# Optimization experiments

Hardware: AMD Instinct MI355X
Metric: run time of the kernel (lower is better)

The kernel has to match this reference:

```python
import jax, jax.numpy as jnp
import numpy as np


def _lstm(x, W, U, b, return_sequences):
    # x: [B,T,F]; W: [F,4H]; U: [H,4H]; b: [4H]. Keras gate order: i,f,c,o.
    B = x.shape[0]
    H = U.shape[0]
    # precompute input projection for all timesteps: [T,B,4H]
    xW = jnp.einsum('btf,fg->tbg', x, W) + b
    h0 = jnp.zeros((B, H), x.dtype)
    c0 = jnp.zeros((B, H), x.dtype)

    def step(carry, xw):
        h, c = carry
        z = xw + h @ U  # [B,4H]
        i, f, g, o = jnp.split(z, 4, axis=-1)
        i = jax.nn.sigmoid(i)
        f = jax.nn.sigmoid(f)
        g = jax.nn.relu(g)      # activation='relu' on candidate
        o = jax.nn.sigmoid(o)
        c = f * c + i * g
        h = o * jax.nn.relu(c)  # activation='relu' on cell output
        return (h, c), h

    (hT, _), hs = jax.lax.scan(step, (h0, c0), xW)
    if return_sequences:
        return jnp.transpose(hs, (1, 0, 2))  # [B,T,H]
    return hT  # [B,H]


def setup_inputs() -> dict:
    key = jax.random.key(0)
    ks = jax.random.split(key, 11)
    B, T, F = 512, 512, 64
    H1, H2, D1, D2 = 128, 64, 25, 1
    s = 0.05  # small weight scale keeps the relu-LSTM recurrence numerically stable
    return {
        'x':   jax.random.normal(ks[0], (B, T, F), jnp.float32),
        'W1':  jax.random.normal(ks[1], (F, 4 * H1), jnp.float32) * s,
        'U1':  jax.random.normal(ks[2], (H1, 4 * H1), jnp.float32) * s,
        'b1':  jnp.zeros((4 * H1,), jnp.float32),
        'W2':  jax.random.normal(ks[3], (H1, 4 * H2), jnp.float32) * s,
        'U2':  jax.random.normal(ks[4], (H2, 4 * H2), jnp.float32) * s,
        'b2':  jnp.zeros((4 * H2,), jnp.float32),
        'Wd1': jax.random.normal(ks[5], (H2, D1), jnp.float32) * s,
        'bd1': jnp.zeros((D1,), jnp.float32),
        'Wd2': jax.random.normal(ks[6], (D1, D2), jnp.float32) * s,
        'bd2': jnp.zeros((D2,), jnp.float32),
    }


def reference(x, W1, U1, b1, W2, U2, b2, Wd1, bd1, Wd2, bd2):
    h = _lstm(x, W1, U1, b1, return_sequences=True)   # [B,T,128]
    h = _lstm(h, W2, U2, b2, return_sequences=False)  # [B,64]
    h = h @ Wd1 + bd1                                  # [B,25]
    return h @ Wd2 + bd2                               # [B,1]
```

## Files before the change

### kernel.cpp

```cpp
#include <hip/hip_runtime.h>
#include <type_traits>

typedef _Float16 f16;
typedef _Float16 f16x4 __attribute__((ext_vector_type(4)));
typedef _Float16 f16x8 __attribute__((ext_vector_type(8)));
typedef float    f32x4 __attribute__((ext_vector_type(4)));

constexpr int TT = 512;
constexpr int FF = 64;
constexpr int H1 = 128;
constexpr int H2 = 64;
constexpr int D1 = 25;
constexpr int S1 = 136;
constexpr int S2 = 72;
constexpr int XC = 8;
constexpr float L2E = 1.44269504088896f;

__device__ __forceinline__ float sigm2(float z) {
    return __builtin_amdgcn_rcpf(1.f + __builtin_amdgcn_exp2f(-z));
}

__device__ __forceinline__ f32x4 mfma16(f16x8 a, f16x8 b, f32x4 c) {
    return __builtin_amdgcn_mfma_f32_16x16x32_f16(a, b, c, 0, 0, 0);
}

__device__ __forceinline__ void gl_lds16(const f16* g, f16* l) {
    __builtin_amdgcn_global_load_lds(
        (const __attribute__((address_space(1))) unsigned int*)g,
        (__attribute__((address_space(3))) unsigned int*)l, 16, 0, 0);
}

__global__ void cvt_x_kernel(const float* __restrict__ x, f16* __restrict__ xh) {
    const size_t i = ((size_t)blockIdx.x * blockDim.x + threadIdx.x) * 4;
    const float4 v = *(const float4*)(x + i);
    f16x4 h; h[0] = (f16)v.x; h[1] = (f16)v.y; h[2] = (f16)v.z; h[3] = (f16)v.w;
    *(f16x4*)(xh + i) = h;
}

__global__ __launch_bounds__(768, 3)
void lstm_pipe9(const f16* __restrict__ xh, const float* __restrict__ W1,
                const float* __restrict__ U1, const float* __restrict__ b1,
                const float* __restrict__ W2, const float* __restrict__ U2,
                const float* __restrict__ b2, const float* __restrict__ Wd1,
                const float* __restrict__ bd1,const float* __restrict__ Wd2,
                const float* __restrict__ bd2, float* __restrict__ out)
{
    const int tid  = threadIdx.x;
    const int w    = tid >> 6;
    const int lane = tid & 63;
    const int quad = lane >> 4;
    const int lid  = lane & 15;
    const int b0   = blockIdx.x * 16;
    const bool isL1 = (w < 8);
    const int  j    = isL1 ? w : (w - 8);

    __shared__ __align__(16) f16 h1b[2][16][S1];
    __shared__ __align__(16) f16 h2b[2][16][S2];
    __shared__ __align__(16) f16 xlds[2][XC * 8 * 16 * 8];
    __shared__ float h2f[16][H2];
    __shared__ float dsh[16][D1];

    for (int i = tid; i < 2 * 16 * S1 / 2; i += 768) ((unsigned*)h1b)[i] = 0u;
    for (int i = tid; i < 2 * 16 * S2 / 2; i += 768) ((unsigned*)h2b)[i] = 0u;

    for (int s = tid; s < XC * 8 * 16; s += 768) {
        const int tl = s >> 7, fs = (s >> 4) & 7, row = s & 15;
        const f16* gp = xh + ((size_t)(b0 + row) * TT + tl) * FF + fs * 8;
        gl_lds16(gp, &xlds[0][(s >> 6) * 512]);
    }

    f16x8 wt[4][6];
    f32x4 bsp[4];
    float cs[4] = {0.f, 0.f, 0.f, 0.f};

    if (isL1) {
#pragma unroll
        for (int g = 0; g < 4; ++g) {
            const float sc = (g == 2) ? 1.f : L2E;
            const int n = 128 * g + 16 * w + lid;
#pragma unroll
            for (int rr = 0; rr < 4; ++rr)
                bsp[g][rr] = b1[128 * g + 16 * w + quad * 4 + rr] * sc;
#pragma unroll
            for (int c = 0; c < 4; ++c) {
                f16x8 f;
#pragma unroll
                for (int e = 0; e < 8; ++e)
                    f[e] = (f16)(U1[(32 * c + quad * 8 + e) * 512 + n] * sc);
                wt[g][c] = f;
            }
#pragma unroll
            for (int c = 0; c < 2; ++c) {
                f16x8 f;
#pragma unroll
                for (int e = 0; e < 8; ++e)
                    f[e] = (f16)(W1[(32 * c + quad * 8 + e) * 512 + n] * sc);
                wt[g][4 + c] = f;
            }
        }
    } else {
#pragma unroll
        for (int g = 0; g < 4; ++g) {
            const float sc = (g == 2) ? 1.f : L2E;
            const int n = 64 * g + 16 * j + lid;
#pragma unroll
            for (int rr = 0; rr < 4; ++rr)
                bsp[g][rr] = b2[64 * g + 16 * j + quad * 4 + rr] * sc;
#pragma unroll
            for (int c = 0; c < 4; ++c) {
                f16x8 f;
#pragma unroll
                for (int e = 0; e < 8; ++e)
                    f[e] = (f16)(W2[(32 * c + quad * 8 + e) * 256 + n] * sc);
                wt[g][c] = f;
            }
#pragma unroll
            for (int c = 0; c < 2; ++c) {
                f16x8 f;
#pragma unroll
                for (int e = 0; e < 8; ++e)
                    f[e] = (f16)(U2[(32 * c + quad * 8 + e) * 256 + n] * sc);
                wt[g][4 + c] = f;
            }
        }
    }
    __syncthreads();

    auto step = [&](auto parc, int i) {
        constexpr int PAR = decltype(parc)::value;
        constexpr int PR = PAR ^ 1;
        constexpr int PW = PAR;
        constexpr int QR = PAR;
        constexpr int QW = PAR ^ 1;
        if (isL1) {
            const f16* xc = &xlds[(i >> 3) & 1][(i & 7) * 1024];
            f16x8 fr0 = *(const f16x8*)&h1b[PR][lid][quad * 8];
            f16x8 fr1 = *(const f16x8*)&h1b[PR][lid][32 + quad * 8];
            f16x8 fr2 = *(const f16x8*)&h1b[PR][lid][64 + quad * 8];
            f16x8 fr3 = *(const f16x8*)&h1b[PR][lid][96 + quad * 8];
            f16x8 xf0 = *(const f16x8*)&xc[(quad * 16 + lid) * 8];
            f16x8 xf1 = *(const f16x8*)&xc[((4 + quad) * 16 + lid) * 8];
            f32x4 acc[4];
#pragma unroll
            for (int g = 0; g < 4; ++g) {
                f32x4 a = mfma16(wt[g][0], fr0, bsp[g]);
                a = mfma16(wt[g][1], fr1, a);
                a = mfma16(wt[g][2], fr2, a);
                a = mfma16(wt[g][3], fr3, a);
                a = mfma16(wt[g][4], xf0, a);
                a = mfma16(wt[g][5], xf1, a);
                acc[g] = a;
            }
            f16x4 hp;
#pragma unroll
            for (int r = 0; r < 4; ++r) {
                const float ig = sigm2(acc[0][r]);
                const float fg = sigm2(acc[1][r]);
                const float gg = fmaxf(acc[2][r], 0.f);
                const float og = sigm2(acc[3][r]);
                const float cc = fg * cs[r] + ig * gg;
                cs[r] = cc;
                hp[r] = (f16)(og * fmaxf(cc, 0.f));
            }
            *(f16x4*)&h1b[PW][lid][16 * w + quad * 4] = hp;
        } else {
            if (i >= 1) {
                f16x8 fr0 = *(const f16x8*)&h1b[PR][lid][quad * 8];
                f16x8 fr1 = *(const f16x8*)&h1b[PR][lid][32 + quad * 8];
                f16x8 fr2 = *(const f16x8*)&h1b[PR][lid][64 + quad * 8];
                f16x8 fr3 = *(const f16x8*)&h1b[PR][lid][96 + quad * 8];
                f16x8 fr4 = *(const f16x8*)&h2b[QR][lid][quad * 8];
                f16x8 fr5 = *(const f16x8*)&h2b[QR][lid][32 + quad * 8];
                f32x4 acc[4];
#pragma unroll
                for (int g = 0; g < 4; ++g) {
                    f32x4 a = mfma16(wt[g][0], fr0, bsp[g]);
                    a = mfma16(wt[g][1], fr1, a);
                    a = mfma16(wt[g][2], fr2, a);
                    a = mfma16(wt[g][3], fr3, a);
                    a = mfma16(wt[g][4], fr4, a);
                    a = mfma16(wt[g][5], fr5, a);
                    acc[g] = a;
                }
                f16x4 hp;
#pragma unroll
                for (int r = 0; r < 4; ++r) {
                    const float ig = sigm2(acc[0][r]);
                    const float fg = sigm2(acc[1][r]);
                    const float gg = fmaxf(acc[2][r], 0.f);
                    const float og = sigm2(acc[3][r]);
                    const float cc = fg * cs[r] + ig * gg;
                    cs[r] = cc;
                    hp[r] = (f16)(og * fmaxf(cc, 0.f));
                }
                *(f16x4*)&h2b[QW][lid][16 * j + quad * 4] = hp;
            }
        }
    };

    for (int ii = 0; ii < TT; ii += 2) {
        if ((ii & (XC - 1)) == 0 && ii + XC < TT) {
            const int nc = (ii >> 3) + 1;
            f16* dst = xlds[nc & 1];
            for (int s = tid; s < XC * 8 * 16; s += 768) {
                const int tl = s >> 7, fs = (s >> 4) & 7, row = s & 15;
                const f16* gp = xh + ((size_t)(b0 + row) * TT + (nc * XC + tl)) * FF + fs * 8;
                gl_lds16(gp, &dst[(s >> 6) * 512]);
            }
        }
        step(std::integral_constant<int, 0>{}, ii);
        __syncthreads();
        step(std::integral_constant<int, 1>{}, ii + 1);
        __syncthreads();
    }

    if (!isL1) {
        f16x8 fr0 = *(const f16x8*)&h1b[1][lid][quad * 8];
        f16x8 fr1 = *(const f16x8*)&h1b[1][lid][32 + quad * 8];
        f16x8 fr2 = *(const f16x8*)&h1b[1][lid][64 + quad * 8];
        f16x8 fr3 = *(const f16x8*)&h1b[1][lid][96 + quad * 8];
        f16x8 fr4 = *(const f16x8*)&h2b[0][lid][quad * 8];
        f16x8 fr5 = *(const f16x8*)&h2b[0][lid][32 + quad * 8];
        f32x4 acc[4];
#pragma unroll
        for (int g = 0; g < 4; ++g) {
            f32x4 a = mfma16(wt[g][0], fr0, bsp[g]);
            a = mfma16(wt[g][1], fr1, a);
            a = mfma16(wt[g][2], fr2, a);
            a = mfma16(wt[g][3], fr3, a);
            a = mfma16(wt[g][4], fr4, a);
            a = mfma16(wt[g][5], fr5, a);
            acc[g] = a;
        }
        float4 ho;
#pragma unroll
        for (int r = 0; r < 4; ++r) {
            const float ig = sigm2(acc[0][r]);
            const float fg = sigm2(acc[1][r]);
            const float gg = fmaxf(acc[2][r], 0.f);
            const float og = sigm2(acc[3][r]);
            const float cc = fg * cs[r] + ig * gg;
            (&ho.x)[r] = og * fmaxf(cc, 0.f);
        }
        *(float4*)&h2f[lid][16 * j + quad * 4] = ho;
    }
    __syncthreads();

    for (int idx = tid; idx < 16 * D1; idx += 768) {
        const int bq = idx / D1, p = idx % D1;
        float d = bd1[p];
#pragma unroll
        for (int k = 0; k < H2; ++k) d += h2f[bq][k] * Wd1[k * D1 + p];
        dsh[bq][p] = d * Wd2[p];
    }
    __syncthreads();
    if (tid < 16) {
        float o = bd2[0];
#pragma unroll
        for (int p = 0; p < D1; ++p) o += dsh[tid][p];
        out[b0 + tid] = o;
    }
}

extern "C" void kernel_launch(void* const* d_in, const int* in_sizes, int n_in,
                              void* d_out, int out_size, void* d_ws, size_t ws_size,
                              hipStream_t stream) {
    (void)in_sizes; (void)n_in; (void)out_size; (void)ws_size;
    const float* x   = (const float*)d_in[0];
    const float* W1  = (const float*)d_in[1];
    const float* U1  = (const float*)d_in[2];
    const float* b1  = (const float*)d_in[3];
    const float* W2  = (const float*)d_in[4];
    const float* U2  = (const float*)d_in[5];
    const float* b2  = (const float*)d_in[6];
    const float* Wd1 = (const float*)d_in[7];
    const float* bd1 = (const float*)d_in[8];
    const float* Wd2 = (const float*)d_in[9];
    const float* bd2 = (const float*)d_in[10];
    float* out = (float*)d_out;
    f16*   xh  = (f16*)d_ws;

    const int nx = 512 * 512 * 64;
    cvt_x_kernel<<<dim3(nx / (256 * 4)), dim3(256), 0, stream>>>(x, xh);
    lstm_pipe9<<<dim3(32), dim3(768), 0, stream>>>(
        xh, W1, U1, b1, W2, U2, b2, Wd1, bd1, Wd2, bd2, out);
}
```

Baseline: 714.2 us.

## Precompute layer-1 input projection in a parallel GEMM kernel before recurrence

Adds a separate highly parallel kernel that computes x*W1+b1 for every timestep and stores it in fp16, in an MFMA-fragment-friendly layout in workspace. The recurrent kernel then only does the U1 matmul per step and prefetches the next step's projection from global memory. This moves the input-projection work off the serial 32-block recurrence and onto the whole GPU. The cost is a 256MB intermediate write and read. The new path runs only when the workspace is large enough, otherwise it falls back to the old path.

Measured after the change: 842.9 us. 1.18x slower.

```diff
diff --git a/kernel.cpp b/kernel.cpp
--- a/kernel.cpp
+++ b/kernel.cpp
@@ -28,6 +28,282 @@
     __builtin_amdgcn_global_load_lds(
         (const __attribute__((address_space(1))) unsigned int*)g,
         (__attribute__((address_space(3))) unsigned int*)l, 16, 0, 0);
+}
+
+__device__ __forceinline__ size_t xw_off(int bg, int t, int w, int quad, int lid) {
+    return ((((size_t)(bg * 512 + t) * 8 + w) * 4 + quad) * 16 + lid) * 16;
+}
+
+__global__ __launch_bounds__(512, 4)
+void xw_gemm(const float* __restrict__ x, const float* __restrict__ W1,
+             const float* __restrict__ b1, f16* __restrict__ xw)
+{
+    const int tid  = threadIdx.x;
+    const int w    = tid >> 6;
+    const int lane = tid & 63;
+    const int quad = lane >> 4;
+    const int lid  = lane & 15;
+    const int bg   = blockIdx.x & 31;
+    const int tc   = blockIdx.x >> 5;
+
+    f16x8 wa[4][2];
+    f32x4 bsp[4];
+#pragma unroll
+    for (int g = 0; g < 4; ++g) {
+        const float sc = (g == 2) ? 1.f : L2E;
+        const int n = 128 * g + 16 * w + lid;
+#pragma unroll
+        for (int rr = 0; rr < 4; ++rr)
+            bsp[g][rr] = b1[128 * g + 16 * w + quad * 4 + rr] * sc;
+#pragma unroll
+        for (int c = 0; c < 2; ++c) {
+            f16x8 f;
+#pragma unroll
+            for (int e = 0; e < 8; ++e)
+                f[e] = (f16)(W1[(32 * c + quad * 8 + e) * 512 + n] * sc);
+            wa[g][c] = f;
+        }
+    }
+
+    for (int tt = 0; tt < 8; ++tt) {
+        const int t = tc * 8 + tt;
+        const float* xr = x + ((size_t)(bg * 16 + lid) * TT + t) * FF + quad * 8;
+        const float4 p0 = *(const float4*)xr;
+        const float4 p1 = *(const float4*)(xr + 4);
+        const float4 p2 = *(const float4*)(xr + 32);
+        const float4 p3 = *(const float4*)(xr + 36);
+        f16x8 xb0, xb1;
+        xb0[0]=(f16)p0.x; xb0[1]=(f16)p0.y; xb0[2]=(f16)p0.z; xb0[3]=(f16)p0.w;
+        xb0[4]=(f16)p1.x; xb0[5]=(f16)p1.y; xb0[6]=(f16)p1.z; xb0[7]=(f16)p1.w;
+        xb1[0]=(f16)p2.x; xb1[1]=(f16)p2.y; xb1[2]=(f16)p2.z; xb1[3]=(f16)p2.w;
+        xb1[4]=(f16)p3.x; xb1[5]=(f16)p3.y; xb1[6]=(f16)p3.z; xb1[7]=(f16)p3.w;
+
+        f32x4 acc[4];
+#pragma unroll
+        for (int g = 0; g < 4; ++g) {
+            f32x4 a = mfma16(wa[g][0], xb0, bsp[g]);
+            acc[g] = mfma16(wa[g][1], xb1, a);
+        }
+        f16x8 s01, s23;
+#pragma unroll
+        for (int r = 0; r < 4; ++r) {
+            s01[r]     = (f16)acc[0][r];
+            s01[4 + r] = (f16)acc[1][r];
+            s23[r]     = (f16)acc[2][r];
+            s23[4 + r] = (f16)acc[3][r];
+        }
+        f16* dst = xw + xw_off(bg, t, w, quad, lid);
+        *(f16x8*)dst = s01;
+        *(f16x8*)(dst + 8) = s23;
+    }
+}
+
+__global__ __launch_bounds__(768, 3)
+void lstm_pipe10(const f16* __restrict__ xw, const float* __restrict__ U1,
+                 const float* __restrict__ W2, const float* __restrict__ U2,
+                 const float* __restrict__ b2, const float* __restrict__ Wd1,
+                 const float* __restrict__ bd1,const float* __restrict__ Wd2,
+                 const float* __restrict__ bd2, float* __restrict__ out)
+{
+    const int tid  = threadIdx.x;
+    const int w    = tid >> 6;
+    const int lane = tid & 63;
+    const int quad = lane >> 4;
+    const int lid  = lane & 15;
+    const int bg   = blockIdx.x;
+    const int b0   = bg * 16;
+    const bool isL1 = (w < 8);
+    const int  j    = isL1 ? w : (w - 8);
+
+    __shared__ __align__(16) f16 h1b[2][16][S1];
+    __shared__ __align__(16) f16 h2b[2][16][S2];
+    __shared__ float h2f[16][H2];
+    __shared__ float dsh[16][D1];
+
+    for (int i = tid; i < 2 * 16 * S1 / 2; i += 768) ((unsigned*)h1b)[i] = 0u;
+    for (int i = tid; i < 2 * 16 * S2 / 2; i += 768) ((unsigned*)h2b)[i] = 0u;
+
+    f16x8 wt[4][6];
+    f32x4 bsp[4];
+    float cs[4] = {0.f, 0.f, 0.f, 0.f};
+    f16x8 xw01, xw23;
+
+    if (isL1) {
+#pragma unroll
+        for (int g = 0; g < 4; ++g) {
+            const float sc = (g == 2) ? 1.f : L2E;
+            const int n = 128 * g + 16 * w + lid;
+#pragma unroll
+            for (int c = 0; c < 4; ++c) {
+                f16x8 f;
+#pragma unroll
+                for (int e = 0; e < 8; ++e)
+                    f[e] = (f16)(U1[(32 * c + quad * 8 + e) * 512 + n] * sc);
+                wt[g][c] = f;
+            }
+        }
+        const f16* p0 = xw + xw_off(bg, 0, w, quad, lid);
+        xw01 = *(const f16x8*)p0;
+        xw23 = *(const f16x8*)(p0 + 8);
+    } else {
+#pragma unroll
+        for (int g = 0; g < 4; ++g) {
+            const float sc = (g == 2) ? 1.f : L2E;
+            const int n = 64 * g + 16 * j + lid;
+#pragma unroll
+            for (int rr = 0; rr < 4; ++rr)
+                bsp[g][rr] = b2[64 * g + 16 * j + quad * 4 + rr] * sc;
+#pragma unroll
+            for (int c = 0; c < 4; ++c) {
+                f16x8 f;
+#pragma unroll
+                for (int e = 0; e < 8; ++e)
+                    f[e] = (f16)(W2[(32 * c + quad * 8 + e) * 256 + n] * sc);
+                wt[g][c] = f;
+            }
+#pragma unroll
+            for (int c = 0; c < 2; ++c) {
+                f16x8 f;
+#pragma unroll
+                for (int e = 0; e < 8; ++e)
+                    f[e] = (f16)(U2[(32 * c + quad * 8 + e) * 256 + n] * sc);
+                wt[g][4 + c] = f;
+            }
+        }
+    }
+    __syncthreads();
+
+    auto step = [&](auto parc, int i) {
+        constexpr int PAR = decltype(parc)::value;
+        constexpr int PR = PAR ^ 1;
+        constexpr int PW = PAR;
+        constexpr int QR = PAR;
+        constexpr int QW = PAR ^ 1;
+        if (isL1) {
+            f16x8 fr0 = *(const f16x8*)&h1b[PR][lid][quad * 8];
+            f16x8 fr1 = *(const f16x8*)&h1b[PR][lid][32 + quad * 8];
+            f16x8 fr2 = *(const f16x8*)&h1b[PR][lid][64 + quad * 8];
+            f16x8 fr3 = *(const f16x8*)&h1b[PR][lid][96 + quad * 8];
+            f32x4 acc[4];
+#pragma unroll
+            for (int r = 0; r < 4; ++r) {
+                acc[0][r] = (float)xw01[r];
+                acc[1][r] = (float)xw01[4 + r];
+                acc[2][r] = (float)xw23[r];
+                acc[3][r] = (float)xw23[4 + r];
+            }
+            if (i + 1 < TT) {
+                const f16* p = xw + xw_off(bg, i + 1, w, quad, lid);
+                xw01 = *(const f16x8*)p;
+                xw23 = *(const f16x8*)(p + 8);
+            }
+#pragma unroll
+            for (int g = 0; g < 4; ++g) {
+                acc[g] = mfma16(wt[g][0], fr0, acc[g]);
+                acc[g] = mfma16(wt[g][1], fr1, acc[g]);
+                acc[g] = mfma16(wt[g][2], fr2, acc[g]);
+                acc[g] = mfma16(wt[g][3], fr3, acc[g]);
+            }
+            f16x4 hp;
+#pragma unroll
+            for (int r = 0; r < 4; ++r) {
+                const float ig = sigm2(acc[0][r]);
+                const float fg = sigm2(acc[1][r]);
+                const float gg = fmaxf(acc[2][r], 0.f);
+                const float og = sigm2(acc[3][r]);
+                const float cc = fg * cs[r] + ig * gg;
+                cs[r] = cc;
+                hp[r] = (f16)(og * fmaxf(cc, 0.f));
+            }
+            *(f16x4*)&h1b[PW][lid][16 * w + quad * 4] = hp;
+        } else {
+            if (i >= 1) {
+                f16x8 fr0 = *(const f16x8*)&h1b[PR][lid][quad * 8];
+                f16x8 fr1 = *(const f16x8*)&h1b[PR][lid][32 + quad * 8];
+                f16x8 fr2 = *(const f16x8*)&h1b[PR][lid][64 + quad * 8];
+                f16x8 fr3 = *(const f16x8*)&h1b[PR][lid][96 + quad * 8];
+                f16x8 fr4 = *(const f16x8*)&h2b[QR][lid][quad * 8];
+                f16x8 fr5 = *(const f16x8*)&h2b[QR][lid][32 + quad * 8];
+                f32x4 acc[4];
+#pragma unroll
+                for (int g = 0; g < 4; ++g) {
+                    f32x4 a = mfma16(wt[g][0], fr0, bsp[g]);
+                    a = mfma16(wt[g][1], fr1, a);
+                    a = mfma16(wt[g][2], fr2, a);
+                    a = mfma16(wt[g][3], fr3, a);
+                    a = mfma16(wt[g][4], fr4, a);
+                    a = mfma16(wt[g][5], fr5, a);
+                    acc[g] = a;
+                }
+                f16x4 hp;
+#pragma unroll
+                for (int r = 0; r < 4; ++r) {
+                    const float ig = sigm2(acc[0][r]);
+                    const float fg = sigm2(acc[1][r]);
+                    const float gg = fmaxf(acc[2][r], 0.f);
+                    const float og = sigm2(acc[3][r]);
+                    const float cc = fg * cs[r] + ig * gg;
+                    cs[r] = cc;
+                    hp[r] = (f16)(og * fmaxf(cc, 0.f));
+                }
+                *(f16x4*)&h2b[QW][lid][16 * j + quad * 4] = hp;
+            }
+        }
+    };
+
+    for (int ii = 0; ii < TT; ii += 2) {
+        step(std::integral_constant<int, 0>{}, ii);
+        __syncthreads();
+        step(std::integral_constant<int, 1>{}, ii + 1);
+        __syncthreads();
+    }
+
+    if (!isL1) {
+        f16x8 fr0 = *(const f16x8*)&h1b[1][lid][quad * 8];
+        f16x8 fr1 = *(const f16x8*)&h1b[1][lid][32 + quad * 8];
+        f16x8 fr2 = *(const f16x8*)&h1b[1][lid][64 + quad * 8];
+        f16x8 fr3 = *(const f16x8*)&h1b[1][lid][96 + quad * 8];
+        f16x8 fr4 = *(const f16x8*)&h2b[0][lid][quad * 8];
+        f16x8 fr5 = *(const f16x8*)&h2b[0][lid][32 + quad * 8];
+        f32x4 acc[4];
+#pragma unroll
+        for (int g = 0; g < 4; ++g) {
+            f32x4 a = mfma16(wt[g][0], fr0, bsp[g]);
+            a = mfma16(wt[g][1], fr1, a);
+            a = mfma16(wt[g][2], fr2, a);
+            a = mfma16(wt[g][3], fr3, a);
+            a = mfma16(wt[g][4], fr4, a);
+            a = mfma16(wt[g][5], fr5, a);
+            acc[g] = a;
+        }
+        float4 ho;
+#pragma unroll
+        for (int r = 0; r < 4; ++r) {
+            const float ig = sigm2(acc[0][r]);
+            const float fg = sigm2(acc[1][r]);
+            const float gg = fmaxf(acc[2][r], 0.f);
+            const float og = sigm2(acc[3][r]);
+            const float cc = fg * cs[r] + ig * gg;
+            (&ho.x)[r] = og * fmaxf(cc, 0.f);
+        }
+        *(float4*)&h2f[lid][16 * j + quad * 4] = ho;
+    }
+    __syncthreads();
+
+    for (int idx = tid; idx < 16 * D1; idx += 768) {
+        const int bq = idx / D1, p = idx % D1;
+        float d = bd1[p];
+#pragma unroll
+        for (int k = 0; k < H2; ++k) d += h2f[bq][k] * Wd1[k * D1 + p];
+        dsh[bq][p] = d * Wd2[p];
+    }
+    __syncthreads();
+    if (tid < 16) {
+        float o = bd2[0];
+#pragma unroll
+        for (int p = 0; p < D1; ++p) o += dsh[tid][p];
+        out[b0 + tid] = o;
+    }
 }
 
 __global__ void cvt_x_kernel(const float* __restrict__ x, f16* __restrict__ xh) {
@@ -265,7 +541,7 @@
 extern "C" void kernel_launch(void* const* d_in, const int* in_sizes, int n_in,
                               void* d_out, int out_size, void* d_ws, size_t ws_size,
                               hipStream_t stream) {
-    (void)in_sizes; (void)n_in; (void)out_size; (void)ws_size;
+    (void)in_sizes; (void)n_in; (void)out_size;
     const float* x   = (const float*)d_in[0];
     const float* W1  = (const float*)d_in[1];
     const float* U1  = (const float*)d_in[2];
@@ -278,10 +554,18 @@
     const float* Wd2 = (const float*)d_in[9];
     const float* bd2 = (const float*)d_in[10];
     float* out = (float*)d_out;
-    f16*   xh  = (f16*)d_ws;
-
-    const int nx = 512 * 512 * 64;
-    cvt_x_kernel<<<dim3(nx / (256 * 4)), dim3(256), 0, stream>>>(x, xh);
-    lstm_pipe9<<<dim3(32), dim3(768), 0, stream>>>(
-        xh, W1, U1, b1, W2, U2, b2, Wd1, bd1, Wd2, bd2, out);
-}
+
+    const size_t need = (size_t)512 * 512 * 512 * sizeof(f16);
+    if (ws_size >= need) {
+        f16* xwbuf = (f16*)d_ws;
+        xw_gemm<<<dim3(2048), dim3(512), 0, stream>>>(x, W1, b1, xwbuf);
+        lstm_pipe10<<<dim3(32), dim3(768), 0, stream>>>(
+            xwbuf, U1, W2, U2, b2, Wd1, bd1, Wd2, bd2, out);
+    } else {
+        f16* xh = (f16*)d_ws;
+        const int nx = 512 * 512 * 64;
+        cvt_x_kernel<<<dim3(nx / (256 * 4)), dim3(256), 0, stream>>>(x, xh);
+        lstm_pipe9<<<dim3(32), dim3(768), 0, stream>>>(
+            xh, W1, U1, b1, W2, U2, b2, Wd1, bd1, Wd2, bd2, out);
+    }
+}
```
